# Performance work log

Hardware: AMD Instinct MI355X
Metric: run time of the kernel (lower is better)

## Reference

```python
import jax, jax.numpy as jnp
import numpy as np

N, E, R = 10000, 320000, 32
IN, H, OUT, REL_IN = 256, 256, 256, 768
GAMMA = 10.0


def _seg_softmax(logits, seg, n):
    # numerically stable softmax over edges grouped by target node
    m = jax.ops.segment_max(logits, seg, num_segments=n)
    e = jnp.exp(logits - m[seg])
    s = jax.ops.segment_sum(e, seg, num_segments=n)
    return e / (s[seg] + 1e-16)


def _rgat_layer(x, src, dst, etype, W, q, k, n):
    # per-relation linear transform of all nodes: [N, R, H]
    xt = jnp.einsum('ni,rio->nro', x, W)
    xj = xt[src, etype]          # [E, H] transformed source feats
    xi = xt[dst, etype]          # [E, H] transformed target feats
    logits = jax.nn.leaky_relu((xi * q[etype]).sum(-1) + (xj * k[etype]).sum(-1), 0.2)
    a = _seg_softmax(logits, dst, n)            # [E]
    return jax.ops.segment_sum(a[:, None] * xj, dst, num_segments=n)  # [N, H]


def setup_inputs() -> dict:
    key = jax.random.key(0)
    ks = jax.random.split(key, 16)
    s = 0.05
    return {
        'x': jax.random.normal(ks[0], (N, IN), jnp.float32),
        'edge_index': jax.random.randint(ks[1], (2, E), 0, N, jnp.int32),
        'edge_type': jax.random.randint(ks[2], (E,), 0, R, jnp.int32),
        'W1': jax.random.normal(ks[3], (R, IN, H), jnp.float32) * s,
        'q1': jax.random.normal(ks[4], (R, H), jnp.float32) * s,
        'k1': jax.random.normal(ks[5], (R, H), jnp.float32) * s,
        'W2': jax.random.normal(ks[6], (R, H, H), jnp.float32) * s,
        'q2': jax.random.normal(ks[7], (R, H), jnp.float32) * s,
        'k2': jax.random.normal(ks[8], (R, H), jnp.float32) * s,
        'lin_w': jax.random.normal(ks[9], (H, OUT), jnp.float32) * s,
        'lin_b': jnp.zeros((OUT,), jnp.float32),
        'rel_bert': jax.random.normal(ks[10], (R, REL_IN), jnp.float32),
        'rel_lin_w': jax.random.normal(ks[11], (REL_IN, H), jnp.float32) * s,
        'rel_lin_b': jnp.zeros((H,), jnp.float32),
    }


def reference(x, edge_index, edge_type, W1, q1, k1, W2, q2, k2,
              lin_w, lin_b, rel_bert, rel_lin_w, rel_lin_b):
    src, dst = edge_index[0], edge_index[1]
    h = jax.nn.relu(_rgat_layer(x, src, dst, edge_type, W1, q1, k1, N))
    h = jax.nn.relu(_rgat_layer(h, src, dst, edge_type, W2, q2, k2, N))
    h = h @ lin_w + lin_b                                   # [N, OUT]
    # relation embeddings (dropout omitted: eval-mode determinism)
    rel = jax.nn.relu(rel_bert @ rel_lin_w + rel_lin_b)     # [R, H]
    # TransE scoring per edge
    diff = h[src] + rel[edge_type] - h[dst]                 # [E, OUT]
    score = GAMMA - jnp.abs(diff).sum(-1)                   # [E]
    return score
```

## Files before the change

kernel.cpp:

```cpp
#include <hip/hip_runtime.h>
#include <hip/hip_bf16.h>
#include <stdint.h>

#define R_ 32
#define H_ 256
#define GAMMA_ 10.0f

typedef __attribute__((ext_vector_type(4))) float f32x4;
typedef __attribute__((ext_vector_type(2))) float f32x2;
typedef __attribute__((ext_vector_type(8))) short bf16x8;

__device__ __forceinline__ unsigned short f2b(float f){
  union { float f; unsigned u; } v; v.f = f;
  unsigned r = v.u + 0x7FFFu + ((v.u >> 16) & 1u);
  return (unsigned short)(r >> 16);
}
__device__ __forceinline__ float b2f(unsigned short h){
  union { unsigned u; float f; } v; v.u = ((unsigned)h) << 16; return v.f;
}

#if __has_builtin(__builtin_amdgcn_cvt_pk_fp8_f32) && __has_builtin(__builtin_amdgcn_cvt_pk_f32_fp8)
#define HWFP8 1
#else
#define HWFP8 0
__device__ __forceinline__ unsigned f2fp8(float f){
  unsigned s = (__float_as_uint(f) >> 24) & 0x80u;
  float a = fminf(fabsf(f), 448.f);
  unsigned b = __float_as_uint(a);
  b += 0x7FFFFu + ((b >> 20) & 1u);
  unsigned code = (((b >> 23) - 120u) << 3) | ((b >> 20) & 7u);
  code = (a < 0.015625f) ? 0u : code;
  return (s | code) & 0xFFu;
}
__device__ __forceinline__ float fp82f(unsigned c){
  unsigned E = (c >> 3) & 15u, m = c & 7u, s = (c >> 7) & 1u;
  unsigned bits = ((E + 120u) << 23) | (m << 20) | (s << 31);
  float v = __uint_as_float(bits);
  return (E == 0) ? 0.f : v;
}
#endif

__device__ __forceinline__ unsigned pack4_fp8(float a0, float a1, float a2, float a3){
#if HWFP8
  unsigned pk = (unsigned)__builtin_amdgcn_cvt_pk_fp8_f32(a0, a1, 0, false);
  pk = (unsigned)__builtin_amdgcn_cvt_pk_fp8_f32(a2, a3, (int)pk, true);
  return pk;
#else
  return f2fp8(a0) | (f2fp8(a1) << 8) | (f2fp8(a2) << 16) | (f2fp8(a3) << 24);
#endif
}
__device__ __forceinline__ f32x4 unpack4_fp8(unsigned w){
#if HWFP8
  f32x2 lo = __builtin_amdgcn_cvt_pk_f32_fp8((int)w, false);
  f32x2 hi = __builtin_amdgcn_cvt_pk_f32_fp8((int)w, true);
  f32x4 r; r[0] = lo[0]; r[1] = lo[1]; r[2] = hi[0]; r[3] = hi[1];
  return r;
#else
  f32x4 r;
  r[0] = fp82f(w & 255u); r[1] = fp82f((w >> 8) & 255u);
  r[2] = fp82f((w >> 16) & 255u); r[3] = fp82f(w >> 24);
  return r;
#endif
}

__global__ __launch_bounds__(256) void prep_kernel(
    const float* __restrict__ x, unsigned short* __restrict__ xb, int n4,
    const float* __restrict__ W1, unsigned short* __restrict__ Wt1,
    const float* __restrict__ W2, unsigned short* __restrict__ Wt2,
    const float* __restrict__ lin_w, unsigned short* __restrict__ linT,
    const float* __restrict__ q1, const float* __restrict__ k1, float* __restrict__ wqkT1,
    const float* __restrict__ q2, const float* __restrict__ k2, float* __restrict__ wqkT2,
    const float* __restrict__ rb, const float* __restrict__ rw,
    const float* __restrict__ rbias, unsigned short* __restrict__ relb,
    const int* __restrict__ srcp, const int* __restrict__ dst, const int* __restrict__ et,
    int* __restrict__ cnt2, int* __restrict__ flagA, int E, int Nn,
    int nb0, int nb_tw, int nb_lin, int nb_wqk, int nb_rel, int nb_hist){
  __shared__ float tile[32][33];
  const int bx = blockIdx.x, t = threadIdx.x;
  const int b0 = nb0, b1 = b0 + nb_tw, b2 = b1 + nb_tw, b3 = b2 + nb_lin;
  const int b4 = b3 + nb_wqk, b5 = b4 + nb_wqk, b6 = b5 + nb_rel;

  if (bx < b0){
    int i = bx * 256 + t;
    if (i < n4){
      float4 v = ((const float4*)x)[i];
      ushort4 o; o.x=f2b(v.x); o.y=f2b(v.y); o.z=f2b(v.z); o.w=f2b(v.w);
      ((ushort4*)xb)[i] = o;
    }
    return;
  }
  if (bx < b3){
    const float* W; unsigned short* Wt; int local;
    if (bx < b1){ W = W1; Wt = Wt1; local = bx - b0; }
    else if (bx < b2){ W = W2; Wt = Wt2; local = bx - b1; }
    else { W = lin_w; Wt = linT; local = bx - b2; }
    int i0 = (local & 7) * 32, o0 = ((local >> 3) & 7) * 32, r = local >> 6;
    int tx = t & 31, ty = t >> 5;
    const float* Wr = W + (size_t)r * 65536;
    for (int rr = ty; rr < 32; rr += 8)
      tile[rr][tx] = Wr[(size_t)(i0 + rr) * 256 + o0 + tx];
    __syncthreads();
    unsigned short* outr = Wt + (size_t)r * 65536;
    for (int rr = ty; rr < 32; rr += 8)
      outr[(size_t)(o0 + rr) * 256 + i0 + tx] = f2b(tile[tx][rr]);
    return;
  }
  if (bx < b5){
    bool first = bx < b4;
    int local = bx - (first ? b3 : b4);
    int w = t >> 6, lane = t & 63;
    int p = local * 4 + w;
    int i = p & 255, r = p >> 8;
    const float* W  = first ? W1 : W2;
    const float* qv = first ? q1 : q2;
    const float* kv = first ? k1 : k2;
    const float* row = W + ((size_t)r * 256 + i) * 256;
    float sq = 0.f, sk = 0.f;
    #pragma unroll
    for (int q4 = 0; q4 < 4; ++q4){
      int o = lane + q4 * 64;
      float wv = row[o];
      sq += wv * qv[r * 256 + o];
      sk += wv * kv[r * 256 + o];
    }
    #pragma unroll
    for (int o = 32; o; o >>= 1){ sq += __shfl_xor(sq, o); sk += __shfl_xor(sk, o); }
    if (!lane){
      float* wq = first ? wqkT1 : wqkT2;
      wq[i * 64 + r] = sq; wq[i * 64 + 32 + r] = sk;
    }
    return;
  }
  if (bx < b6){
    int r = bx - b5, h = t;
    float acc = rbias[h];
    const float* br = rb + (size_t)r * 768;
    for (int i = 0; i < 768; ++i) acc += br[i] * rw[(size_t)i * 256 + h];
    relb[r * 256 + h] = f2b(fmaxf(acc, 0.f));
    return;
  }
  {
    int e = (bx - b6) * 256 + t;
    if (e < E){
      int d = dst[e], r = et[e];
      atomicAdd(&cnt2[(d >> 5) * 1024 + (d & 31) * 32 + r], 1);
      flagA[r * Nn + srcp[e]] = 1;
    }
  }
}

__global__ void totred_kernel(const int* __restrict__ cnt2, int* __restrict__ tot,
                              const int* __restrict__ flagA, int* __restrict__ tot2, int nblk1){
  __shared__ int red[256];
  int blk = blockIdx.x, t = threadIdx.x;
  const int* srcb = (blk < nblk1) ? (cnt2 + (size_t)blk * 1024) : (flagA + (size_t)(blk - nblk1) * 1024);
  int* dstb = (blk < nblk1) ? (tot + blk) : (tot2 + blk - nblk1);
  int s = 0;
  #pragma unroll
  for (int q = 0; q < 4; ++q) s += srcb[q * 256 + t];
  red[t] = s; __syncthreads();
  for (int o = 128; o; o >>= 1){ if (t < o) red[t] += red[t + o]; __syncthreads(); }
  if (!t) *dstb = red[0];
}
__device__ void scan_body(const int* deg, int* off, int n){
  __shared__ int carry;
  __shared__ int buf[1024];
  if (threadIdx.x == 0) carry = 0;
  __syncthreads();
  for (int base = 0; base < n; base += 1024){
    int i = base + threadIdx.x;
    int v = (i < n) ? deg[i] : 0;
    buf[threadIdx.x] = v; __syncthreads();
    for (int o = 1; o < 1024; o <<= 1){
      int t = (threadIdx.x >= o) ? buf[threadIdx.x - o] : 0;
      __syncthreads();
      buf[threadIdx.x] += t;
      __syncthreads();
    }
    if (i < n) off[i] = carry + buf[threadIdx.x] - v;
    __syncthreads();
    if (threadIdx.x == 1023) carry += buf[1023];
    __syncthreads();
  }
  if (threadIdx.x == 0) off[n] = carry;
  __syncthreads();
}
__global__ void scan_kernel(const int* __restrict__ d1, int* __restrict__ o1, int n1,
                            const int* __restrict__ d2, int* __restrict__ o2, int n2){
  scan_body(d1, o1, n1);
  scan_body(d2, o2, n2);
}
__global__ __launch_bounds__(256) void ps2scan_kernel(
    const int* __restrict__ cnt2, const int* __restrict__ base1, int* __restrict__ ps2, int nblk1,
    const int* __restrict__ flagA, const int* __restrict__ base2, int* __restrict__ ps3, int nblk2){
  __shared__ int sb[1024];
  int blk = blockIdx.x, t = threadIdx.x;
  const bool first = blk < nblk1;
  const int lb = first ? blk : blk - nblk1;
  const int* srcb = first ? (cnt2 + (size_t)lb * 1024) : (flagA + (size_t)lb * 1024);
  int* dstb = first ? (ps2 + (size_t)lb * 1024) : (ps3 + (size_t)lb * 1024);
  const int* base = first ? base1 : base2;
  int orig[4];
  #pragma unroll
  for (int q = 0; q < 4; ++q){ int i = q * 256 + t; orig[q] = srcb[i]; sb[i] = orig[q]; }
  __syncthreads();
  for (int o = 1; o < 1024; o <<= 1){
    int v[4];
    #pragma unroll
    for (int q = 0; q < 4; ++q){ int i = q * 256 + t; v[q] = (i >= o) ? sb[i - o] : 0; }
    __syncthreads();
    #pragma unroll
    for (int q = 0; q < 4; ++q){ int i = q * 256 + t; sb[i] += v[q]; }
    __syncthreads();
  }
  int b = base[lb];
  #pragma unroll
  for (int q = 0; q < 4; ++q){ int i = q * 256 + t; dstb[i] = b + sb[i] - orig[q]; }
  if (lb == 0 && t == 0){
    if (first) ps2[(size_t)nblk1 * 1024] = base1[nblk1];
    else       ps3[(size_t)nblk2 * 1024] = base2[nblk2];
  }
}
__global__ void nodelist_kernel(const int* __restrict__ flagA, const int* __restrict__ ps3,
                                int* __restrict__ nodelist, int ntot, int Nn){
  int i = blockIdx.x * 256 + threadIdx.x;
  if (i < ntot && flagA[i]) nodelist[ps3[i]] = i % Nn;
}
__global__ void scatter2_kernel(const int* __restrict__ src, const int* __restrict__ dst,
                                const int* __restrict__ et, const int* __restrict__ ps2,
                                const int* __restrict__ ps3, int* __restrict__ cur2,
                                int* __restrict__ es_src, int* __restrict__ es_row, int E, int Nn){
  int e = blockIdx.x * 256 + threadIdx.x;
  if (e >= E) return;
  int d = dst[e], r = et[e], s = src[e];
  int key = (d >> 5) * 1024 + (d & 31) * 32 + r;
  int pos = ps2[key] + atomicAdd(&cur2[key], 1);
  es_src[pos] = s;
  es_row[pos] = ps3[(size_t)r * Nn + s];
}

__global__ void qdot_kernel(const unsigned short* __restrict__ xb, const float* __restrict__ wqkT,
                            float* __restrict__ qdot, float* __restrict__ kdot, int n){
  __shared__ float xrow[4][256];
  int w = threadIdx.x >> 6, lane = threadIdx.x & 63;
  int node = blockIdx.x * 4 + w;
  if (node >= n) return;
  ushort4 v = ((const ushort4*)(xb + (size_t)node * 256))[lane];
  float* xr = xrow[w];
  xr[lane * 4 + 0] = b2f(v.x);
  xr[lane * 4 + 1] = b2f(v.y);
  xr[lane * 4 + 2] = b2f(v.z);
  xr[lane * 4 + 3] = b2f(v.w);
  float acc = 0.f;
  #pragma unroll 8
  for (int kk = 0; kk < 256; ++kk)
    acc = fmaf(xr[kk], wqkT[kk * 64 + lane], acc);
  if (lane < 32) qdot[node * 32 + lane] = acc;
  else           kdot[node * 32 + lane - 32] = acc;
}

template<int MODE>
__global__ __launch_bounds__(512) void gemm3_kernel(
    const unsigned short* __restrict__ A, const unsigned short* __restrict__ Bt,
    void* __restrict__ Cv, const float* __restrict__ bias, int M, int MT,
    const int* __restrict__ nodelist, const int* __restrict__ ps3, int Nn){
  __shared__ unsigned short As[2][128 * 64];
  __shared__ unsigned short Bs[2][256 * 64];
  __shared__ int rowsL[128];
  const int bx = blockIdx.x;
  const int r  = (MODE == 0) ? bx / MT : 0;
  const int mb = (MODE == 0) ? bx % MT : bx;
  int u0 = 0, u1 = M;
  if (MODE == 0){
    u0 = ps3[(size_t)r * Nn];
    u1 = ps3[(size_t)(r + 1) * Nn];
    if (mb * 128 >= u1 - u0) return;
  }
  const int tid = threadIdx.x, lane = tid & 63, wid = tid >> 6;
  const int wm = (wid >> 2) * 64;
  const int wn = (wid & 3) * 64;
  const int lg = lane >> 4, lr = lane & 15;
  const unsigned short* Brel = Bt + (size_t)r * 65536;

  if (tid < 128){
    if (MODE == 0){
      int cr = u0 + mb * 128 + tid;
      if (cr >= u1) cr = u1 - 1;
      rowsL[tid] = nodelist[cr];
    } else {
      int g = mb * 128 + tid; if (g >= M) g = M - 1;
      rowsL[tid] = g;
    }
  }
  __syncthreads();

  f32x4 acc[4][4];
  #pragma unroll
  for (int i = 0; i < 4; ++i)
    #pragma unroll
    for (int j = 0; j < 4; ++j) acc[i][j] = (f32x4)0.0f;

  auto stage = [&](int buf, int kt){
    #pragma unroll
    for (int q = 0; q < 2; ++q){
      int ci = q * 512 + tid;
      int row = ci >> 3, p = ci & 7;
      int gch = p ^ (row & 7);
      const unsigned short* ga = A + (size_t)rowsL[row] * 256 + kt * 64 + gch * 8;
      __builtin_amdgcn_global_load_lds((const __attribute__((address_space(1))) void*)ga,
          (__attribute__((address_space(3))) void*)(As[buf] + (size_t)ci * 8), 16, 0, 0);
    }
    #pragma unroll
    for (int q = 0; q < 4; ++q){
      int ci = q * 512 + tid;
      int row = ci >> 3, p = ci & 7;
      int gch = p ^ (row & 7);
      const unsigned short* gb = Brel + (size_t)row * 256 + kt * 64 + gch * 8;
      __builtin_amdgcn_global_load_lds((const __attribute__((address_space(1))) void*)gb,
          (__attribute__((address_space(3))) void*)(Bs[buf] + (size_t)ci * 8), 16, 0, 0);
    }
  };

  stage(0, 0);
  __syncthreads();

  for (int kt = 0; kt < 4; ++kt){
    const int cur = kt & 1;
    if (kt < 3) stage(cur ^ 1, kt + 1);
    #pragma unroll
    for (int kk = 0; kk < 2; ++kk){
      bf16x8 af[4], bg[4];
      #pragma unroll
      for (int mi = 0; mi < 4; ++mi){
        int row = wm + mi * 16 + lr;
        int pc = (lg + kk * 4) ^ (row & 7);
        af[mi] = *(const bf16x8*)&As[cur][row * 64 + pc * 8];
      }
      #pragma unroll
      for (int ni = 0; ni < 4; ++ni){
        int row = wn + ni * 16 + lr;
        int pc = (lg + kk * 4) ^ (row & 7);
        bg[ni] = *(const bf16x8*)&Bs[cur][row * 64 + pc * 8];
      }
      #pragma unroll
      for (int mi = 0; mi < 4; ++mi)
        #pragma unroll
        for (int ni = 0; ni < 4; ++ni)
          acc[mi][ni] = __builtin_amdgcn_mfma_f32_16x16x32_bf16(af[mi], bg[ni], acc[mi][ni], 0, 0, 0);
    }
    __syncthreads();
  }

  if (MODE == 0){
    #pragma unroll
    for (int mi = 0; mi < 4; ++mi){
      #pragma unroll
      for (int j = 0; j < 4; ++j){
        int rowloc = wm + mi * 16 + lg * 4 + j;
        int cr = u0 + mb * 128 + rowloc;
        if (cr < u1){
          unsigned pk = pack4_fp8(acc[mi][0][j], acc[mi][1][j], acc[mi][2][j], acc[mi][3][j]);
          *(unsigned*)((unsigned char*)Cv + (size_t)cr * 256 + wn + lr * 4) = pk;
        }
      }
    }
  } else {
    #pragma unroll
    for (int mi = 0; mi < 4; ++mi){
      #pragma unroll
      for (int j = 0; j < 4; ++j){
        int rowm = mb * 128 + wm + mi * 16 + lg * 4 + j;
        if (rowm >= M) continue;
        #pragma unroll
        for (int ni = 0; ni < 4; ++ni){
          int col = wn + ni * 16 + lr;
          ((unsigned short*)Cv)[(size_t)rowm * H_ + col] = f2b(acc[mi][ni][j] + bias[col]);
        }
      }
    }
  }
}

__global__ void attn_agg_kernel(const unsigned char* __restrict__ xt8, const float* __restrict__ qdot,
                                const float* __restrict__ kdot, const int* __restrict__ ps2,
                                const int* __restrict__ es_src, const int* __restrict__ es_row,
                                float* __restrict__ a, unsigned short* __restrict__ hout, int n){
  int w = threadIdx.x >> 6, lane = threadIdx.x & 63;
  int node = blockIdx.x * 4 + w;
  if (node >= n) return;
  int kb = (node >> 5) * 1024 + (node & 31) * 32;
  int s = 0, e = 0;
  float qd = 0.f;
  if (lane < 32){
    s = ps2[kb + lane]; e = ps2[kb + lane + 1];
    qd = qdot[node * 32 + lane];
  }
  float m = -1e30f;
  for (int j = s; j < e; ++j){
    float z = qd + kdot[es_src[j] * 32 + lane];
    z = (z > 0.f) ? z : 0.2f * z;
    a[j] = z;
    m = fmaxf(m, z);
  }
  #pragma unroll
  for (int o = 32; o; o >>= 1) m = fmaxf(m, __shfl_xor(m, o));
  float sum = 0.f;
  for (int j = s; j < e; ++j){
    float ez = __expf(a[j] - m);
    a[j] = ez; sum += ez;
  }
  #pragma unroll
  for (int o = 32; o; o >>= 1) sum += __shfl_xor(sum, o);
  float inv = 1.0f / (sum + 1e-16f);
  int s0 = ps2[kb], s1 = ps2[kb + 32];
  float a0 = 0.f, a1 = 0.f, a2 = 0.f, a3 = 0.f;
  int j = s0;
  for (; j + 2 <= s1; j += 2){
    int r0 = es_row[j], r1 = es_row[j+1];
    float w0 = a[j], w1 = a[j+1];
    unsigned v0 = ((const unsigned*)(xt8 + (size_t)r0 * 256))[lane];
    unsigned v1 = ((const unsigned*)(xt8 + (size_t)r1 * 256))[lane];
    f32x4 d0 = unpack4_fp8(v0), d1 = unpack4_fp8(v1);
    a0 += w0*d0[0] + w1*d1[0];
    a1 += w0*d0[1] + w1*d1[1];
    a2 += w0*d0[2] + w1*d1[2];
    a3 += w0*d0[3] + w1*d1[3];
  }
  for (; j < s1; ++j){
    float wv = a[j];
    unsigned v = ((const unsigned*)(xt8 + (size_t)es_row[j] * 256))[lane];
    f32x4 d = unpack4_fp8(v);
    a0 = fmaf(wv, d[0], a0);
    a1 = fmaf(wv, d[1], a1);
    a2 = fmaf(wv, d[2], a2);
    a3 = fmaf(wv, d[3], a3);
  }
  int cb = ((lane & 48) << 2) + (lane & 15);
  unsigned short* hn = hout + (size_t)node * H_;
  hn[cb +  0] = f2b(fmaxf(a0 * inv, 0.f));
  hn[cb + 16] = f2b(fmaxf(a1 * inv, 0.f));
  hn[cb + 32] = f2b(fmaxf(a2 * inv, 0.f));
  hn[cb + 48] = f2b(fmaxf(a3 * inv, 0.f));
}

__global__ void score_kernel(const unsigned short* __restrict__ hb, const unsigned short* __restrict__ relb,
                             const int* __restrict__ src_a, const int* __restrict__ dst_a,
                             const int* __restrict__ et_a, float* __restrict__ out, int E){
  int e = blockIdx.x * 4 + (threadIdx.x >> 6);
  int lane = threadIdx.x & 63;
  if (e >= E) return;
  int s = src_a[e], d = dst_a[e], r = et_a[e];
  ushort4 a4 = ((const ushort4*)(hb + (size_t)s * H_))[lane];
  ushort4 b4 = ((const ushort4*)(hb + (size_t)d * H_))[lane];
  ushort4 r4 = ((const ushort4*)(relb + (size_t)r * H_))[lane];
  float sum = fabsf(b2f(a4.x) + b2f(r4.x) - b2f(b4.x))
            + fabsf(b2f(a4.y) + b2f(r4.y) - b2f(b4.y))
            + fabsf(b2f(a4.z) + b2f(r4.z) - b2f(b4.z))
            + fabsf(b2f(a4.w) + b2f(r4.w) - b2f(b4.w));
  #pragma unroll
  for (int o = 32; o; o >>= 1) sum += __shfl_xor(sum, o);
  if (!lane) out[e] = GAMMA_ - sum;
}

extern "C" void kernel_launch(void* const* d_in, const int* in_sizes, int n_in,
                              void* d_out, int out_size, void* d_ws, size_t ws_size,
                              hipStream_t stream){
  const float* x         = (const float*)d_in[0];
  const int*   edge_idx  = (const int*)d_in[1];
  const int*   edge_type = (const int*)d_in[2];
  const float* W1        = (const float*)d_in[3];
  const float* q1        = (const float*)d_in[4];
  const float* k1        = (const float*)d_in[5];
  const float* W2        = (const float*)d_in[6];
  const float* q2        = (const float*)d_in[7];
  const float* k2        = (const float*)d_in[8];
  const float* lin_w     = (const float*)d_in[9];
  const float* lin_b     = (const float*)d_in[10];
  const float* rel_bert  = (const float*)d_in[11];
  const float* rel_lin_w = (const float*)d_in[12];
  const float* rel_lin_b = (const float*)d_in[13];
  float* score = (float*)d_out;

  const int Nn = in_sizes[0] / H_;
  const int E  = in_sizes[1] / 2;
  const int* src_a = edge_idx;
  const int* dst_a = edge_idx + E;
  const int NBLK   = (Nn + 31) / 32;
  const int NBINS  = NBLK * 1024;
  const int NB2    = (R_ * Nn + 1023) / 1024;
  const int NBINS2 = NB2 * 1024;

  char* ws = (char*)d_ws;
  size_t cur_off = 0;
  auto carve = [&](size_t bytes)->char*{
    char* p = ws + cur_off;
    cur_off += (bytes + 255) & ~(size_t)255;
    return p;
  };
  unsigned char*  xt8  = (unsigned char*)carve((size_t)Nn * R_ * H_);
  unsigned short* xb   = (unsigned short*)carve((size_t)Nn * H_ * 2);
  unsigned short* h1   = (unsigned short*)carve((size_t)Nn * H_ * 2);
  unsigned short* h2   = (unsigned short*)carve((size_t)Nn * H_ * 2);
  unsigned short* outb = (unsigned short*)carve((size_t)Nn * H_ * 2);
  unsigned short* Wt1  = (unsigned short*)carve((size_t)R_ * 65536 * 2);
  unsigned short* Wt2  = (unsigned short*)carve((size_t)R_ * 65536 * 2);
  unsigned short* linT = (unsigned short*)carve(65536 * 2);
  unsigned short* relb = (unsigned short*)carve(R_ * H_ * 2);
  float* wqkT1 = (float*)carve(64 * H_ * 4);
  float* wqkT2 = (float*)carve(64 * H_ * 4);
  float* qdot  = (float*)carve((size_t)Nn * R_ * 4);
  float* kdot  = (float*)carve((size_t)Nn * R_ * 4);
  int* cnt2    = (int*)carve((size_t)NBINS * 4);
  int* cur2    = (int*)carve((size_t)NBINS * 4);
  int* flagA   = (int*)carve((size_t)NBINS2 * 4);
  int* tot     = (int*)carve((size_t)NBLK * 4);
  int* tot2    = (int*)carve((size_t)NB2 * 4);
  int* baseA   = (int*)carve((size_t)(NBLK + 1) * 4);
  int* base2   = (int*)carve((size_t)(NB2 + 1) * 4);
  int* ps2     = (int*)carve((size_t)(NBINS + 1) * 4);
  int* ps3     = (int*)carve((size_t)(NBINS2 + 1) * 4);
  int* nodelist= (int*)carve((size_t)(R_ * Nn) * 4);
  int* es_src  = (int*)carve((size_t)E * 4);
  int* es_row  = (int*)carve((size_t)E * 4);
  float* attn  = (float*)carve((size_t)E * 4);
  (void)ws_size; (void)n_in; (void)out_size;

  const int mt = (Nn + 127) / 128;
  const int nqd = (Nn + 3) / 4;

  const int n4 = Nn * H_ / 4;
  const int nb0 = (n4 + 255) / 256, nb_tw = 2048, nb_lin = 64, nb_wqk = 2048, nb_rel = 32;
  const int nb_hist = (E + 255) / 256;
  const int nprep = nb0 + 2 * nb_tw + nb_lin + 2 * nb_wqk + nb_rel + nb_hist;

  hipMemsetAsync(cnt2, 0, (size_t)NBINS * 4, stream);
  hipMemsetAsync(cur2, 0, (size_t)NBINS * 4, stream);
  hipMemsetAsync(flagA, 0, (size_t)NBINS2 * 4, stream);

  prep_kernel<<<nprep, 256, 0, stream>>>(
      x, xb, n4, W1, Wt1, W2, Wt2, lin_w, linT,
      q1, k1, wqkT1, q2, k2, wqkT2,
      rel_bert, rel_lin_w, rel_lin_b, relb,
      src_a, dst_a, edge_type, cnt2, flagA, E, Nn,
      nb0, nb_tw, nb_lin, nb_wqk, nb_rel, nb_hist);

  totred_kernel<<<NBLK + NB2, 256, 0, stream>>>(cnt2, tot, flagA, tot2, NBLK);
  scan_kernel<<<1, 1024, 0, stream>>>(tot, baseA, NBLK, tot2, base2, NB2);
  ps2scan_kernel<<<NBLK + NB2, 256, 0, stream>>>(cnt2, baseA, ps2, NBLK, flagA, base2, ps3, NB2);
  nodelist_kernel<<<(NBINS2 + 255) / 256, 256, 0, stream>>>(flagA, ps3, nodelist, R_ * Nn, Nn);
  scatter2_kernel<<<(E + 255) / 256, 256, 0, stream>>>(src_a, dst_a, edge_type, ps2, ps3, cur2, es_src, es_row, E, Nn);

  gemm3_kernel<0><<<R_ * mt, 512, 0, stream>>>(xb, Wt1, xt8, nullptr, Nn, mt, nodelist, ps3, Nn);
  qdot_kernel<<<nqd, 256, 0, stream>>>(xb, wqkT1, qdot, kdot, Nn);
  attn_agg_kernel<<<nqd, 256, 0, stream>>>(xt8, qdot, kdot, ps2, es_src, es_row, attn, h1, Nn);

  gemm3_kernel<0><<<R_ * mt, 512, 0, stream>>>(h1, Wt2, xt8, nullptr, Nn, mt, nodelist, ps3, Nn);
  qdot_kernel<<<nqd, 256, 0, stream>>>(h1, wqkT2, qdot, kdot, Nn);
  attn_agg_kernel<<<nqd, 256, 0, stream>>>(xt8, qdot, kdot, ps2, es_src, es_row, attn, h2, Nn);

  gemm3_kernel<1><<<mt, 512, 0, stream>>>(h2, linT, outb, lin_b, Nn, mt, nullptr, nullptr, Nn);
  score_kernel<<<(E + 3) / 4, 256, 0, stream>>>(outb, relb, src_a, dst_a, edge_type, score, E);
}
```

Before: 384.9 us.

## Score edges per destination node using sorted edge lists, fp32 relation table

The TransE scoring kernel now walks edges grouped by destination node through the existing CSR-like ordering. It loads the destination row once per wave and reuses it across all incoming edges, with two edges processed per iteration. Each edge's original index is stored so its score is written back to the right output slot. The relation embeddings are kept in fp32 rather than bf16. In exchange, the scatter pass writes two extra per-edge arrays, and the output writes become scattered.

```diff
diff --git a/kernel.cpp b/kernel.cpp
--- a/kernel.cpp
+++ b/kernel.cpp
@@ -71,7 +71,7 @@
     const float* __restrict__ q1, const float* __restrict__ k1, float* __restrict__ wqkT1,
     const float* __restrict__ q2, const float* __restrict__ k2, float* __restrict__ wqkT2,
     const float* __restrict__ rb, const float* __restrict__ rw,
-    const float* __restrict__ rbias, unsigned short* __restrict__ relb,
+    const float* __restrict__ rbias, float* __restrict__ relf,
     const int* __restrict__ srcp, const int* __restrict__ dst, const int* __restrict__ et,
     int* __restrict__ cnt2, int* __restrict__ flagA, int E, int Nn,
     int nb0, int nb_tw, int nb_lin, int nb_wqk, int nb_rel, int nb_hist){
@@ -136,7 +136,7 @@
     float acc = rbias[h];
     const float* br = rb + (size_t)r * 768;
     for (int i = 0; i < 768; ++i) acc += br[i] * rw[(size_t)i * 256 + h];
-    relb[r * 256 + h] = f2b(fmaxf(acc, 0.f));
+    relf[r * 256 + h] = fmaxf(acc, 0.f);
     return;
   }
   {
@@ -229,7 +229,8 @@
 __global__ void scatter2_kernel(const int* __restrict__ src, const int* __restrict__ dst,
                                 const int* __restrict__ et, const int* __restrict__ ps2,
                                 const int* __restrict__ ps3, int* __restrict__ cur2,
-                                int* __restrict__ es_src, int* __restrict__ es_row, int E, int Nn){
+                                int* __restrict__ es_src, int* __restrict__ es_row,
+                                int* __restrict__ es_et, int* __restrict__ es_eid, int E, int Nn){
   int e = blockIdx.x * 256 + threadIdx.x;
   if (e >= E) return;
   int d = dst[e], r = et[e], s = src[e];
@@ -237,6 +238,8 @@
   int pos = ps2[key] + atomicAdd(&cur2[key], 1);
   es_src[pos] = s;
   es_row[pos] = ps3[(size_t)r * Nn + s];
+  es_et[pos]  = r;
+  es_eid[pos] = e;
 }
 
 __global__ void qdot_kernel(const unsigned short* __restrict__ xb, const float* __restrict__ wqkT,
@@ -443,23 +446,43 @@
   hn[cb + 48] = f2b(fmaxf(a3 * inv, 0.f));
 }
 
-__global__ void score_kernel(const unsigned short* __restrict__ hb, const unsigned short* __restrict__ relb,
-                             const int* __restrict__ src_a, const int* __restrict__ dst_a,
-                             const int* __restrict__ et_a, float* __restrict__ out, int E){
-  int e = blockIdx.x * 4 + (threadIdx.x >> 6);
-  int lane = threadIdx.x & 63;
-  if (e >= E) return;
-  int s = src_a[e], d = dst_a[e], r = et_a[e];
-  ushort4 a4 = ((const ushort4*)(hb + (size_t)s * H_))[lane];
-  ushort4 b4 = ((const ushort4*)(hb + (size_t)d * H_))[lane];
-  ushort4 r4 = ((const ushort4*)(relb + (size_t)r * H_))[lane];
-  float sum = fabsf(b2f(a4.x) + b2f(r4.x) - b2f(b4.x))
-            + fabsf(b2f(a4.y) + b2f(r4.y) - b2f(b4.y))
-            + fabsf(b2f(a4.z) + b2f(r4.z) - b2f(b4.z))
-            + fabsf(b2f(a4.w) + b2f(r4.w) - b2f(b4.w));
-  #pragma unroll
-  for (int o = 32; o; o >>= 1) sum += __shfl_xor(sum, o);
-  if (!lane) out[e] = GAMMA_ - sum;
+__global__ void score2_kernel(const unsigned short* __restrict__ hb, const float* __restrict__ relf,
+                              const int* __restrict__ ps2, const int* __restrict__ es_src,
+                              const int* __restrict__ es_et, const int* __restrict__ es_eid,
+                              float* __restrict__ out, int n){
+  int w = threadIdx.x >> 6, lane = threadIdx.x & 63;
+  int node = blockIdx.x * 4 + w;
+  if (node >= n) return;
+  int kb = (node >> 5) * 1024 + (node & 31) * 32;
+  int s0 = ps2[kb], s1 = ps2[kb + 32];
+  ushort4 hd4 = ((const ushort4*)(hb + (size_t)node * H_))[lane];
+  float d0 = b2f(hd4.x), d1 = b2f(hd4.y), d2 = b2f(hd4.z), d3 = b2f(hd4.w);
+  int j = s0;
+  for (; j + 2 <= s1; j += 2){
+    int sA = es_src[j],   rA = es_et[j],   eA = es_eid[j];
+    int sB = es_src[j+1], rB = es_et[j+1], eB = es_eid[j+1];
+    ushort4 hA = ((const ushort4*)(hb + (size_t)sA * H_))[lane];
+    ushort4 hB = ((const ushort4*)(hb + (size_t)sB * H_))[lane];
+    float4 vA = ((const float4*)(relf + rA * H_))[lane];
+    float4 vB = ((const float4*)(relf + rB * H_))[lane];
+    float sumA = fabsf(b2f(hA.x) + vA.x - d0) + fabsf(b2f(hA.y) + vA.y - d1)
+               + fabsf(b2f(hA.z) + vA.z - d2) + fabsf(b2f(hA.w) + vA.w - d3);
+    float sumB = fabsf(b2f(hB.x) + vB.x - d0) + fabsf(b2f(hB.y) + vB.y - d1)
+               + fabsf(b2f(hB.z) + vB.z - d2) + fabsf(b2f(hB.w) + vB.w - d3);
+    #pragma unroll
+    for (int o = 32; o; o >>= 1){ sumA += __shfl_xor(sumA, o); sumB += __shfl_xor(sumB, o); }
+    if (!lane){ out[eA] = GAMMA_ - sumA; out[eB] = GAMMA_ - sumB; }
+  }
+  for (; j < s1; ++j){
+    int sc = es_src[j], r = es_et[j], eid = es_eid[j];
+    ushort4 hs = ((const ushort4*)(hb + (size_t)sc * H_))[lane];
+    float4 rv = ((const float4*)(relf + r * H_))[lane];
+    float sum = fabsf(b2f(hs.x) + rv.x - d0) + fabsf(b2f(hs.y) + rv.y - d1)
+              + fabsf(b2f(hs.z) + rv.z - d2) + fabsf(b2f(hs.w) + rv.w - d3);
+    #pragma unroll
+    for (int o = 32; o; o >>= 1) sum += __shfl_xor(sum, o);
+    if (!lane) out[eid] = GAMMA_ - sum;
+  }
 }
 
 extern "C" void kernel_launch(void* const* d_in, const int* in_sizes, int n_in,
@@ -505,7 +528,7 @@
   unsigned short* Wt1  = (unsigned short*)carve((size_t)R_ * 65536 * 2);
   unsigned short* Wt2  = (unsigned short*)carve((size_t)R_ * 65536 * 2);
   unsigned short* linT = (unsigned short*)carve(65536 * 2);
-  unsigned short* relb = (unsigned short*)carve(R_ * H_ * 2);
+  float* relf  = (float*)carve((size_t)R_ * H_ * 4);
   float* wqkT1 = (float*)carve(64 * H_ * 4);
   float* wqkT2 = (float*)carve(64 * H_ * 4);
   float* qdot  = (float*)carve((size_t)Nn * R_ * 4);
@@ -522,6 +545,8 @@
   int* nodelist= (int*)carve((size_t)(R_ * Nn) * 4);
   int* es_src  = (int*)carve((size_t)E * 4);
   int* es_row  = (int*)carve((size_t)E * 4);
+  int* es_et   = (int*)carve((size_t)E * 4);
+  int* es_eid  = (int*)carve((size_t)E * 4);
   float* attn  = (float*)carve((size_t)E * 4);
   (void)ws_size; (void)n_in; (void)out_size;
 
@@ -540,7 +565,7 @@
   prep_kernel<<<nprep, 256, 0, stream>>>(
       x, xb, n4, W1, Wt1, W2, Wt2, lin_w, linT,
       q1, k1, wqkT1, q2, k2, wqkT2,
-      rel_bert, rel_lin_w, rel_lin_b, relb,
+      rel_bert, rel_lin_w, rel_lin_b, relf,
       src_a, dst_a, edge_type, cnt2, flagA, E, Nn,
       nb0, nb_tw, nb_lin, nb_wqk, nb_rel, nb_hist);
 
@@ -548,7 +573,8 @@
   scan_kernel<<<1, 1024, 0, stream>>>(tot, baseA, NBLK, tot2, base2, NB2);
   ps2scan_kernel<<<NBLK + NB2, 256, 0, stream>>>(cnt2, baseA, ps2, NBLK, flagA, base2, ps3, NB2);
   nodelist_kernel<<<(NBINS2 + 255) / 256, 256, 0, stream>>>(flagA, ps3, nodelist, R_ * Nn, Nn);
-  scatter2_kernel<<<(E + 255) / 256, 256, 0, stream>>>(src_a, dst_a, edge_type, ps2, ps3, cur2, es_src, es_row, E, Nn);
+  scatter2_kernel<<<(E + 255) / 256, 256, 0, stream>>>(src_a, dst_a, edge_type, ps2, ps3, cur2,
+                                                       es_src, es_row, es_et, es_eid, E, Nn);
 
   gemm3_kernel<0><<<R_ * mt, 512, 0, stream>>>(xb, Wt1, xt8, nullptr, Nn, mt, nodelist, ps3, Nn);
   qdot_kernel<<<nqd, 256, 0, stream>>>(xb, wqkT1, qdot, kdot, Nn);
@@ -559,5 +585,5 @@
   attn_agg_kernel<<<nqd, 256, 0, stream>>>(xt8, qdot, kdot, ps2, es_src, es_row, attn, h2, Nn);
 
   gemm3_kernel<1><<<mt, 512, 0, stream>>>(h2, linT, outb, lin_b, Nn, mt, nullptr, nullptr, Nn);
-  score_kernel<<<(E + 3) / 4, 256, 0, stream>>>(outb, relb, src_a, dst_a, edge_type, score, E);
-}
+  score2_kernel<<<nqd, 256, 0, stream>>>(outb, relf, ps2, es_src, es_et, es_eid, score, Nn);
+}
```

After: 388.5 us. No clear change (+0.9%).
